# Kernel tuning notes

Hardware: AMD Instinct MI355X
Metric: run time of the kernel (lower is better)

Reference implementation:

```python
import jax, jax.numpy as jnp
import numpy as np

N = 100000          # active sites
C_IN = 256          # inplanes == outplanes
C_MID = 64          # innerplanes
K = 9               # 3x3 kernel offsets (2D)


def setup_inputs() -> dict:
    key = jax.random.key(0)
    ks = jax.random.split(key, 12)
    features = jax.random.normal(ks[0], (N, C_IN), dtype=jnp.float32)
    # submanifold rulebook: for each active site, index of active neighbor per
    # kernel offset; sentinel N = no active neighbor, center (offset 4) = self
    idx = jax.random.randint(ks[1], (N, K), 0, N, dtype=jnp.int32)
    drop = jax.random.uniform(ks[2], (N, K)) < 0.3
    idx = jnp.where(drop, jnp.int32(N), idx)
    neighbor_idx = idx.at[:, 4].set(jnp.arange(N, dtype=jnp.int32))
    s = 0.05
    return {
        "features": features,
        "neighbor_idx": neighbor_idx,
        "w1": jax.random.normal(ks[3], (C_IN, C_MID), dtype=jnp.float32) * s,
        "scale1": jnp.ones((C_MID,), jnp.float32),
        "bias1": jnp.zeros((C_MID,), jnp.float32),
        "w2": jax.random.normal(ks[4], (K, C_MID, C_MID), dtype=jnp.float32) * s,
        "scale2": jnp.ones((C_MID,), jnp.float32),
        "bias2": jnp.zeros((C_MID,), jnp.float32),
        "w3": jax.random.normal(ks[5], (C_MID, C_IN), dtype=jnp.float32) * s,
        "scale3": jnp.ones((C_IN,), jnp.float32),
        "bias3": jnp.zeros((C_IN,), jnp.float32),
    }


def reference(features, neighbor_idx, w1, scale1, bias1, w2, scale2, bias2,
              w3, scale3, bias3):
    # conv1: 1x1 submanifold conv == per-site matmul; affine BN; ReLU
    out = jax.nn.relu(features @ w1 * scale1 + bias1)            # [N, C_MID]
    # conv2: 3x3 submanifold conv via rulebook gather-matmul-accumulate
    padded = jnp.concatenate([out, jnp.zeros((1, C_MID), out.dtype)], axis=0)
    gathered = padded[neighbor_idx]                               # [N, K, C_MID]
    out = jnp.einsum('nkc,kcd->nd', gathered, w2)                 # [N, C_MID]
    out = jax.nn.relu(out * scale2 + bias2)
    # conv3: 1x1 conv; affine BN; residual add (downsample=None); ReLU
    out = out @ w3 * scale3 + bias3 + features                    # [N, C_IN]
    return jax.nn.relu(out)
```

## Files before the change

kernel.cpp:

```cpp
#include <hip/hip_runtime.h>
#include <stdint.h>

#define C_IN 256
#define C_MID 64
#define KOFF 9

typedef __attribute__((ext_vector_type(8))) short bf16x8;
typedef __attribute__((ext_vector_type(4))) short short4v;
typedef __attribute__((ext_vector_type(4))) float f32x4;
typedef __attribute__((ext_vector_type(4))) float float4v;

__device__ inline unsigned short f2bf(float f) {
    union { float f; unsigned u; } x; x.f = f;
    unsigned r = x.u + 0x7FFFu + ((x.u >> 16) & 1u);
    return (unsigned short)(r >> 16);
}

__global__ void prep_kernel(const float* __restrict__ w1, const float* __restrict__ s1,
                            const float* __restrict__ w2, const float* __restrict__ s2,
                            const float* __restrict__ w3, const float* __restrict__ s3,
                            unsigned short* __restrict__ w1t,
                            unsigned short* __restrict__ w2t,
                            unsigned short* __restrict__ w3t,
                            unsigned short* __restrict__ zrow) {
    int tid = blockIdx.x * blockDim.x + threadIdx.x;
    int stride = gridDim.x * blockDim.x;
    for (int i = tid; i < C_MID * C_IN; i += stride) {
        int n = i / C_IN, k = i % C_IN;
        w1t[i] = f2bf(w1[k * C_MID + n] * s1[n]);
    }
    for (int i = tid; i < KOFF * C_MID * C_MID; i += stride) {
        int k = i / (C_MID * C_MID);
        int r = i % (C_MID * C_MID);
        int d = r / C_MID, c = r % C_MID;
        w2t[i] = f2bf(w2[(k * C_MID + c) * C_MID + d] * s2[d]);
    }
    for (int i = tid; i < C_IN * C_MID; i += stride) {
        int e = i / C_MID, c = i % C_MID;
        w3t[i] = f2bf(w3[c * C_IN + e] * s3[e]);
    }
    for (int i = tid; i < C_MID; i += stride) zrow[i] = 0;
}

__global__ __launch_bounds__(256, 4) void conv1_kernel(
    const float* __restrict__ feat, const unsigned short* __restrict__ w1t,
    const float* __restrict__ b1, unsigned short* __restrict__ out1, int N)
{
    __shared__ __align__(16) unsigned short sW1[16384];

    int t = threadIdx.x;
    int wave = t >> 6;
    int lane = t & 63;
    int l15 = lane & 15;
    int quad = lane >> 4;
    int row_tile = blockIdx.x * 64;
    int site = row_tile + wave * 16 + l15;
    int sitec = site < N ? site : (N - 1);

    const bf16x8* w1c = reinterpret_cast<const bf16x8*>(w1t);
    bf16x8* sW1c = reinterpret_cast<bf16x8*>(sW1);
#pragma unroll
    for (int it = 0; it < 8; ++it) {
        int s = it * 256 + t;
        int l = s & 15, ct = (s >> 4) & 3, q = (s >> 6) & 3, kk = s >> 8;
        sW1c[s] = w1c[(ct * 16 + l) * 32 + kk * 4 + q];
    }

    float4v fr[16];
#pragma unroll
    for (int kk = 0; kk < 8; ++kk) {
        const float4v* p = reinterpret_cast<const float4v*>(
            feat + (size_t)sitec * C_IN + kk * 32 + quad * 8);
        fr[kk * 2] = p[0];
        fr[kk * 2 + 1] = p[1];
    }
    __builtin_amdgcn_sched_barrier(0);
    __syncthreads();

    f32x4 acc[4] = {};
#pragma unroll
    for (int kk = 0; kk < 8; ++kk) {
        union { unsigned short s[8]; bf16x8 v; } ua;
#pragma unroll
        for (int j = 0; j < 4; ++j) {
            ua.s[j] = f2bf(fr[kk * 2][j]);
            ua.s[4 + j] = f2bf(fr[kk * 2 + 1][j]);
        }
#pragma unroll
        for (int ct = 0; ct < 4; ++ct) {
            bf16x8 fa = sW1c[((kk * 4 + quad) * 4 + ct) * 16 + l15];
            acc[ct] = __builtin_amdgcn_mfma_f32_16x16x32_bf16(fa, ua.v, acc[ct], 0, 0, 0);
        }
    }
    if (site < N) {
#pragma unroll
        for (int ct = 0; ct < 4; ++ct) {
            const float4v* bp = reinterpret_cast<const float4v*>(b1 + ct * 16 + quad * 4);
            float4v bb = bp[0];
            union { unsigned short s[4]; short4v v; } o;
#pragma unroll
            for (int reg = 0; reg < 4; ++reg)
                o.s[reg] = f2bf(fmaxf(acc[ct][reg] + bb[reg], 0.f));
            *reinterpret_cast<short4v*>(out1 + (size_t)site * C_MID + ct * 16 + quad * 4) = o.v;
        }
    }
}

__global__ __launch_bounds__(256, 2) void conv23_kernel(
    const float* __restrict__ feat, const int* __restrict__ nbr,
    const unsigned short* __restrict__ out1, const unsigned short* __restrict__ w2t,
    const float* __restrict__ b2, const unsigned short* __restrict__ w3t,
    const float* __restrict__ b3, float* __restrict__ out, int N)
{
    __shared__ __align__(16) unsigned short sWB[36864];
    __shared__ int sNbr[64 * KOFF];

    int t = threadIdx.x;
    int wave = t >> 6;
    int lane = t & 63;
    int l15 = lane & 15;
    int quad = lane >> 4;
    int row_tile = blockIdx.x * 64;
    int site = row_tile + wave * 16 + l15;
    int sitec = site < N ? site : (N - 1);

    bf16x8* sWBc = reinterpret_cast<bf16x8*>(sWB);

    const bf16x8* w2c = reinterpret_cast<const bf16x8*>(w2t);
#pragma unroll
    for (int it = 0; it < 18; ++it) {
        int s = it * 256 + t;
        int l = s & 15, ct = (s >> 4) & 3, q = (s >> 6) & 3, kk = (s >> 8) & 1, k = s >> 9;
        sWBc[s] = w2c[k * 512 + (ct * 16 + l) * 8 + kk * 4 + q];
    }
#pragma unroll
    for (int i = 0; i < 3; ++i) {
        int j = i * 256 + t;
        if (j < 64 * KOFF) {
            int g = row_tile * KOFF + j;
            sNbr[j] = (g < N * KOFF) ? nbr[g] : N;
        }
    }
    __syncthreads();

    int rt = wave * 16 + l15;
    int nb[KOFF];
#pragma unroll
    for (int k = 0; k < KOFF; ++k) nb[k] = sNbr[rt * KOFF + k];

    bf16x8 ga[KOFF][2];
#pragma unroll
    for (int k = 0; k < KOFF; ++k) {
        const bf16x8* pg = reinterpret_cast<const bf16x8*>(out1 + (size_t)nb[k] * C_MID + quad * 8);
        ga[k][0] = pg[0];
        ga[k][1] = pg[4];
    }
    float4v rf[16];
#pragma unroll
    for (int c2 = 0; c2 < 16; ++c2)
        rf[c2] = *reinterpret_cast<const float4v*>(
            feat + (size_t)sitec * C_IN + c2 * 16 + quad * 4);
    __builtin_amdgcn_sched_barrier(0);

    f32x4 acc2[4] = {};
#pragma unroll
    for (int k = 0; k < KOFF; ++k) {
#pragma unroll
        for (int kk = 0; kk < 2; ++kk) {
#pragma unroll
            for (int ct = 0; ct < 4; ++ct) {
                bf16x8 fa = sWBc[((k * 2 + kk) * 4 + quad) * 64 + ct * 16 + l15];
                acc2[ct] = __builtin_amdgcn_mfma_f32_16x16x32_bf16(fa, ga[k][kk], acc2[ct], 0, 0, 0);
            }
        }
    }
    __syncthreads();

    unsigned short* mid = &sWB[31744];
#pragma unroll
    for (int ct = 0; ct < 4; ++ct) {
        const float4v* bp = reinterpret_cast<const float4v*>(b2 + ct * 16 + quad * 4);
        float4v bb = bp[0];
        union { unsigned short s[4]; short4v v; } o;
#pragma unroll
        for (int reg = 0; reg < 4; ++reg)
            o.s[reg] = f2bf(fmaxf(acc2[ct][reg] + bb[reg], 0.f));
        *reinterpret_cast<short4v*>(&mid[(wave * 16 + l15) * 80 + ct * 16 + quad * 4]) = o.v;
    }
    const bf16x8* w3c = reinterpret_cast<const bf16x8*>(w3t);
#pragma unroll
    for (int it = 0; it < 8; ++it) {
        int s = it * 256 + t;
        int l = s & 15, c2 = (s >> 4) & 15, q = (s >> 8) & 3, kk = (s >> 10) & 1;
        sWBc[s] = w3c[(c2 * 16 + l) * 8 + kk * 4 + q];
    }
    __syncthreads();

    f32x4 acc3[16] = {};
#pragma unroll
    for (int kk = 0; kk < 2; ++kk) {
        bf16x8 fb = *reinterpret_cast<const bf16x8*>(
            &mid[(wave * 16 + l15) * 80 + kk * 32 + quad * 8]);
#pragma unroll
        for (int c2 = 0; c2 < 16; ++c2) {
            bf16x8 fa = sWBc[((kk * 4 + quad) * 16 + c2) * 16 + l15];
            acc3[c2] = __builtin_amdgcn_mfma_f32_16x16x32_bf16(fa, fb, acc3[c2], 0, 0, 0);
        }
    }
    if (site < N) {
#pragma unroll
        for (int c2 = 0; c2 < 16; ++c2) {
            const float4v* bp = reinterpret_cast<const float4v*>(b3 + c2 * 16 + quad * 4);
            float4v bb = bp[0];
            float4v o;
#pragma unroll
            for (int reg = 0; reg < 4; ++reg)
                o[reg] = fmaxf(acc3[c2][reg] + bb[reg] + rf[c2][reg], 0.f);
            *reinterpret_cast<float4v*>(out + (size_t)site * C_IN + c2 * 16 + quad * 4) = o;
        }
    }
}

extern "C" void kernel_launch(void* const* d_in, const int* in_sizes, int n_in,
                              void* d_out, int out_size, void* d_ws, size_t ws_size,
                              hipStream_t stream) {
    const float* feat = (const float*)d_in[0];
    const int*   nbr  = (const int*)d_in[1];
    const float* w1   = (const float*)d_in[2];
    const float* s1   = (const float*)d_in[3];
    const float* b1   = (const float*)d_in[4];
    const float* w2   = (const float*)d_in[5];
    const float* s2   = (const float*)d_in[6];
    const float* b2   = (const float*)d_in[7];
    const float* w3   = (const float*)d_in[8];
    const float* s3   = (const float*)d_in[9];
    const float* b3   = (const float*)d_in[10];
    float* out = (float*)d_out;
    int N = in_sizes[0] / C_IN;

    char* ws = (char*)d_ws;
    unsigned short* w1t  = (unsigned short*)(ws);
    unsigned short* w2t  = (unsigned short*)(ws + 32768);
    unsigned short* w3t  = (unsigned short*)(ws + 32768 + 73728);
    unsigned short* out1 = (unsigned short*)(ws + 139264);

    prep_kernel<<<80, 256, 0, stream>>>(w1, s1, w2, s2, w3, s3, w1t, w2t, w3t,
                                        out1 + (size_t)N * C_MID);
    int nblk = (N + 63) / 64;
    conv1_kernel<<<nblk, 256, 0, stream>>>(feat, w1t, b1, out1, N);
    conv23_kernel<<<nblk, 256, 0, stream>>>(feat, nbr, out1, w2t, b2, w3t, b3, out, N);
}
```

Measured before the change: 263.8 us.

## Double conv23 block size and split conv3 into halves to cut register pressure

The conv23 kernel now processes 128 sites per 512-thread block, so the 72KB shared weight load is amortized over twice as many sites. Residual feature loads are split in two halves, and conv3 accumulation is done in two 8-tile passes, to lower live registers and allow launch_bounds(512,4). The mid buffer moves to a smaller-stride region. The risk is spilling or lower occupancy if the register target cannot be met, and larger blocks make tail effects coarser.

```diff
diff --git a/kernel.cpp b/kernel.cpp
--- a/kernel.cpp
+++ b/kernel.cpp
@@ -106,44 +106,43 @@
     }
 }
 
-__global__ __launch_bounds__(256, 2) void conv23_kernel(
+__global__ __launch_bounds__(512, 4) void conv23_kernel(
     const float* __restrict__ feat, const int* __restrict__ nbr,
     const unsigned short* __restrict__ out1, const unsigned short* __restrict__ w2t,
     const float* __restrict__ b2, const unsigned short* __restrict__ w3t,
     const float* __restrict__ b3, float* __restrict__ out, int N)
 {
     __shared__ __align__(16) unsigned short sWB[36864];
-    __shared__ int sNbr[64 * KOFF];
+    __shared__ int sNbr[128 * KOFF];
 
     int t = threadIdx.x;
     int wave = t >> 6;
     int lane = t & 63;
     int l15 = lane & 15;
     int quad = lane >> 4;
-    int row_tile = blockIdx.x * 64;
-    int site = row_tile + wave * 16 + l15;
+    int rt = wave * 16 + l15;
+    int site = blockIdx.x * 128 + rt;
     int sitec = site < N ? site : (N - 1);
 
     bf16x8* sWBc = reinterpret_cast<bf16x8*>(sWB);
 
     const bf16x8* w2c = reinterpret_cast<const bf16x8*>(w2t);
 #pragma unroll
-    for (int it = 0; it < 18; ++it) {
-        int s = it * 256 + t;
+    for (int it = 0; it < 9; ++it) {
+        int s = it * 512 + t;
         int l = s & 15, ct = (s >> 4) & 3, q = (s >> 6) & 3, kk = (s >> 8) & 1, k = s >> 9;
         sWBc[s] = w2c[k * 512 + (ct * 16 + l) * 8 + kk * 4 + q];
     }
 #pragma unroll
     for (int i = 0; i < 3; ++i) {
-        int j = i * 256 + t;
-        if (j < 64 * KOFF) {
-            int g = row_tile * KOFF + j;
+        int j = i * 512 + t;
+        if (j < 128 * KOFF) {
+            int g = blockIdx.x * 128 * KOFF + j;
             sNbr[j] = (g < N * KOFF) ? nbr[g] : N;
         }
     }
     __syncthreads();
 
-    int rt = wave * 16 + l15;
     int nb[KOFF];
 #pragma unroll
     for (int k = 0; k < KOFF; ++k) nb[k] = sNbr[rt * KOFF + k];
@@ -155,11 +154,6 @@
         ga[k][0] = pg[0];
         ga[k][1] = pg[4];
     }
-    float4v rf[16];
-#pragma unroll
-    for (int c2 = 0; c2 < 16; ++c2)
-        rf[c2] = *reinterpret_cast<const float4v*>(
-            feat + (size_t)sitec * C_IN + c2 * 16 + quad * 4);
     __builtin_amdgcn_sched_barrier(0);
 
     f32x4 acc2[4] = {};
@@ -174,49 +168,73 @@
             }
         }
     }
-    __syncthreads();
-
-    unsigned short* mid = &sWB[31744];
+    float4v b2r[4];
+#pragma unroll
+    for (int ct = 0; ct < 4; ++ct)
+        b2r[ct] = *reinterpret_cast<const float4v*>(b2 + ct * 16 + quad * 4);
+    float4v rfA[8], b3A[8];
+#pragma unroll
+    for (int c8 = 0; c8 < 8; ++c8) {
+        rfA[c8] = *reinterpret_cast<const float4v*>(
+            feat + (size_t)sitec * C_IN + c8 * 16 + quad * 4);
+        b3A[c8] = *reinterpret_cast<const float4v*>(b3 + c8 * 16 + quad * 4);
+    }
+    __builtin_amdgcn_sched_barrier(0);
+    __syncthreads();
+
+    unsigned short* mid = &sWB[16384];
 #pragma unroll
     for (int ct = 0; ct < 4; ++ct) {
-        const float4v* bp = reinterpret_cast<const float4v*>(b2 + ct * 16 + quad * 4);
-        float4v bb = bp[0];
         union { unsigned short s[4]; short4v v; } o;
 #pragma unroll
         for (int reg = 0; reg < 4; ++reg)
-            o.s[reg] = f2bf(fmaxf(acc2[ct][reg] + bb[reg], 0.f));
-        *reinterpret_cast<short4v*>(&mid[(wave * 16 + l15) * 80 + ct * 16 + quad * 4]) = o.v;
+            o.s[reg] = f2bf(fmaxf(acc2[ct][reg] + b2r[ct][reg], 0.f));
+        *reinterpret_cast<short4v*>(&mid[rt * 72 + ct * 16 + quad * 4]) = o.v;
     }
     const bf16x8* w3c = reinterpret_cast<const bf16x8*>(w3t);
 #pragma unroll
-    for (int it = 0; it < 8; ++it) {
-        int s = it * 256 + t;
+    for (int it = 0; it < 4; ++it) {
+        int s = it * 512 + t;
         int l = s & 15, c2 = (s >> 4) & 15, q = (s >> 8) & 3, kk = (s >> 10) & 1;
         sWBc[s] = w3c[(c2 * 16 + l) * 8 + kk * 4 + q];
     }
     __syncthreads();
 
-    f32x4 acc3[16] = {};
-#pragma unroll
-    for (int kk = 0; kk < 2; ++kk) {
-        bf16x8 fb = *reinterpret_cast<const bf16x8*>(
-            &mid[(wave * 16 + l15) * 80 + kk * 32 + quad * 8]);
-#pragma unroll
-        for (int c2 = 0; c2 < 16; ++c2) {
-            bf16x8 fa = sWBc[((kk * 4 + quad) * 16 + c2) * 16 + l15];
-            acc3[c2] = __builtin_amdgcn_mfma_f32_16x16x32_bf16(fa, fb, acc3[c2], 0, 0, 0);
-        }
-    }
-    if (site < N) {
-#pragma unroll
-        for (int c2 = 0; c2 < 16; ++c2) {
-            const float4v* bp = reinterpret_cast<const float4v*>(b3 + c2 * 16 + quad * 4);
-            float4v bb = bp[0];
-            float4v o;
-#pragma unroll
-            for (int reg = 0; reg < 4; ++reg)
-                o[reg] = fmaxf(acc3[c2][reg] + bb[reg] + rf[c2][reg], 0.f);
-            *reinterpret_cast<float4v*>(out + (size_t)site * C_IN + c2 * 16 + quad * 4) = o;
+    float4v rfB[8], b3B[8];
+#pragma unroll
+    for (int c8 = 0; c8 < 8; ++c8) {
+        rfB[c8] = *reinterpret_cast<const float4v*>(
+            feat + (size_t)sitec * C_IN + (8 + c8) * 16 + quad * 4);
+        b3B[c8] = *reinterpret_cast<const float4v*>(b3 + (8 + c8) * 16 + quad * 4);
+    }
+    __builtin_amdgcn_sched_barrier(0);
+
+#pragma unroll
+    for (int half = 0; half < 2; ++half) {
+        f32x4 acc3[8] = {};
+#pragma unroll
+        for (int kk = 0; kk < 2; ++kk) {
+            bf16x8 fb = *reinterpret_cast<const bf16x8*>(
+                &mid[rt * 72 + kk * 32 + quad * 8]);
+#pragma unroll
+            for (int c8 = 0; c8 < 8; ++c8) {
+                int c2 = half * 8 + c8;
+                bf16x8 fa = sWBc[((kk * 4 + quad) * 16 + c2) * 16 + l15];
+                acc3[c8] = __builtin_amdgcn_mfma_f32_16x16x32_bf16(fa, fb, acc3[c8], 0, 0, 0);
+            }
+        }
+        if (site < N) {
+#pragma unroll
+            for (int c8 = 0; c8 < 8; ++c8) {
+                int c2 = half * 8 + c8;
+                float4v bb = half ? b3B[c8] : b3A[c8];
+                float4v rr = half ? rfB[c8] : rfA[c8];
+                float4v o;
+#pragma unroll
+                for (int reg = 0; reg < 4; ++reg)
+                    o[reg] = fmaxf(acc3[c8][reg] + bb[reg] + rr[reg], 0.f);
+                *reinterpret_cast<float4v*>(out + (size_t)site * C_IN + c2 * 16 + quad * 4) = o;
+            }
         }
     }
 }
@@ -246,7 +264,6 @@
 
     prep_kernel<<<80, 256, 0, stream>>>(w1, s1, w2, s2, w3, s3, w1t, w2t, w3t,
                                         out1 + (size_t)N * C_MID);
-    int nblk = (N + 63) / 64;
-    conv1_kernel<<<nblk, 256, 0, stream>>>(feat, w1t, b1, out1, N);
-    conv23_kernel<<<nblk, 256, 0, stream>>>(feat, nbr, out1, w2t, b2, w3t, b3, out, N);
-}
+    conv1_kernel<<<(N + 63) / 64, 256, 0, stream>>>(feat, w1t, b1, out1, N);
+    conv23_kernel<<<(N + 127) / 128, 512, 0, stream>>>(feat, nbr, out1, w2t, b2, w3t, b3, out, N);
+}
```

Result: slower. 287.9 us (+9.1%).

## Split conv2 weight staging into two LDS phases and defer residual loads

Applied to the files above, without the earlier changes.

The conv23 kernel now stages the 3x3 weights in two chunks (offsets 0-4, then 5-8) so the shared buffer shrinks from about 72KB to about 42KB. The aim is to allow more blocks per CU. The residual feature loads move after the conv2 MMAs to cut register pressure during the gather/MMA phase, and conv1 splits its feature loads into two halves. In exchange it adds extra syncthreads and a second global weight load per block, and the mid tile padding changes from 80 to 72.

```diff
diff --git a/kernel.cpp b/kernel.cpp
--- a/kernel.cpp
+++ b/kernel.cpp
@@ -53,8 +53,7 @@
     int lane = t & 63;
     int l15 = lane & 15;
     int quad = lane >> 4;
-    int row_tile = blockIdx.x * 64;
-    int site = row_tile + wave * 16 + l15;
+    int site = blockIdx.x * 64 + wave * 16 + l15;
     int sitec = site < N ? site : (N - 1);
 
     const bf16x8* w1c = reinterpret_cast<const bf16x8*>(w1t);
@@ -66,25 +65,35 @@
         sW1c[s] = w1c[(ct * 16 + l) * 32 + kk * 4 + q];
     }
 
-    float4v fr[16];
-#pragma unroll
-    for (int kk = 0; kk < 8; ++kk) {
+    float4v fr0[8];
+#pragma unroll
+    for (int kk = 0; kk < 4; ++kk) {
         const float4v* p = reinterpret_cast<const float4v*>(
             feat + (size_t)sitec * C_IN + kk * 32 + quad * 8);
-        fr[kk * 2] = p[0];
-        fr[kk * 2 + 1] = p[1];
-    }
-    __builtin_amdgcn_sched_barrier(0);
-    __syncthreads();
+        fr0[kk * 2] = p[0];
+        fr0[kk * 2 + 1] = p[1];
+    }
+    __builtin_amdgcn_sched_barrier(0);
+    __syncthreads();
+
+    float4v fr1[8];
+#pragma unroll
+    for (int kk = 0; kk < 4; ++kk) {
+        const float4v* p = reinterpret_cast<const float4v*>(
+            feat + (size_t)sitec * C_IN + (kk + 4) * 32 + quad * 8);
+        fr1[kk * 2] = p[0];
+        fr1[kk * 2 + 1] = p[1];
+    }
+    __builtin_amdgcn_sched_barrier(0);
 
     f32x4 acc[4] = {};
 #pragma unroll
-    for (int kk = 0; kk < 8; ++kk) {
+    for (int kk = 0; kk < 4; ++kk) {
         union { unsigned short s[8]; bf16x8 v; } ua;
 #pragma unroll
         for (int j = 0; j < 4; ++j) {
-            ua.s[j] = f2bf(fr[kk * 2][j]);
-            ua.s[4 + j] = f2bf(fr[kk * 2 + 1][j]);
+            ua.s[j] = f2bf(fr0[kk * 2][j]);
+            ua.s[4 + j] = f2bf(fr0[kk * 2 + 1][j]);
         }
 #pragma unroll
         for (int ct = 0; ct < 4; ++ct) {
@@ -92,11 +101,24 @@
             acc[ct] = __builtin_amdgcn_mfma_f32_16x16x32_bf16(fa, ua.v, acc[ct], 0, 0, 0);
         }
     }
+#pragma unroll
+    for (int kk = 0; kk < 4; ++kk) {
+        union { unsigned short s[8]; bf16x8 v; } ua;
+#pragma unroll
+        for (int j = 0; j < 4; ++j) {
+            ua.s[j] = f2bf(fr1[kk * 2][j]);
+            ua.s[4 + j] = f2bf(fr1[kk * 2 + 1][j]);
+        }
+#pragma unroll
+        for (int ct = 0; ct < 4; ++ct) {
+            bf16x8 fa = sW1c[(((kk + 4) * 4 + quad) * 4 + ct) * 16 + l15];
+            acc[ct] = __builtin_amdgcn_mfma_f32_16x16x32_bf16(fa, ua.v, acc[ct], 0, 0, 0);
+        }
+    }
     if (site < N) {
 #pragma unroll
         for (int ct = 0; ct < 4; ++ct) {
-            const float4v* bp = reinterpret_cast<const float4v*>(b1 + ct * 16 + quad * 4);
-            float4v bb = bp[0];
+            float4v bb = *reinterpret_cast<const float4v*>(b1 + ct * 16 + quad * 4);
             union { unsigned short s[4]; short4v v; } o;
 #pragma unroll
             for (int reg = 0; reg < 4; ++reg)
@@ -112,7 +134,7 @@
     const float* __restrict__ b2, const unsigned short* __restrict__ w3t,
     const float* __restrict__ b3, float* __restrict__ out, int N)
 {
-    __shared__ __align__(16) unsigned short sWB[36864];
+    __shared__ __align__(16) unsigned short sWB[21504];
     __shared__ int sNbr[64 * KOFF];
 
     int t = threadIdx.x;
@@ -120,15 +142,15 @@
     int lane = t & 63;
     int l15 = lane & 15;
     int quad = lane >> 4;
-    int row_tile = blockIdx.x * 64;
-    int site = row_tile + wave * 16 + l15;
+    int rt = wave * 16 + l15;
+    int site = blockIdx.x * 64 + rt;
     int sitec = site < N ? site : (N - 1);
 
     bf16x8* sWBc = reinterpret_cast<bf16x8*>(sWB);
-
     const bf16x8* w2c = reinterpret_cast<const bf16x8*>(w2t);
-#pragma unroll
-    for (int it = 0; it < 18; ++it) {
+
+#pragma unroll
+    for (int it = 0; it < 10; ++it) {
         int s = it * 256 + t;
         int l = s & 15, ct = (s >> 4) & 3, q = (s >> 6) & 3, kk = (s >> 8) & 1, k = s >> 9;
         sWBc[s] = w2c[k * 512 + (ct * 16 + l) * 8 + kk * 4 + q];
@@ -137,13 +159,12 @@
     for (int i = 0; i < 3; ++i) {
         int j = i * 256 + t;
         if (j < 64 * KOFF) {
-            int g = row_tile * KOFF + j;
+            int g = blockIdx.x * 64 * KOFF + j;
             sNbr[j] = (g < N * KOFF) ? nbr[g] : N;
         }
     }
     __syncthreads();
 
-    int rt = wave * 16 + l15;
     int nb[KOFF];
 #pragma unroll
     for (int k = 0; k < KOFF; ++k) nb[k] = sNbr[rt * KOFF + k];
@@ -155,16 +176,11 @@
         ga[k][0] = pg[0];
         ga[k][1] = pg[4];
     }
-    float4v rf[16];
-#pragma unroll
-    for (int c2 = 0; c2 < 16; ++c2)
-        rf[c2] = *reinterpret_cast<const float4v*>(
-            feat + (size_t)sitec * C_IN + c2 * 16 + quad * 4);
     __builtin_amdgcn_sched_barrier(0);
 
     f32x4 acc2[4] = {};
 #pragma unroll
-    for (int k = 0; k < KOFF; ++k) {
+    for (int k = 0; k < 5; ++k) {
 #pragma unroll
         for (int kk = 0; kk < 2; ++kk) {
 #pragma unroll
@@ -176,16 +192,42 @@
     }
     __syncthreads();
 
-    unsigned short* mid = &sWB[31744];
+#pragma unroll
+    for (int it = 0; it < 8; ++it) {
+        int s = it * 256 + t;
+        int l = s & 15, ct = (s >> 4) & 3, q = (s >> 6) & 3, kk = (s >> 8) & 1, k2 = s >> 9;
+        sWBc[s] = w2c[(5 + k2) * 512 + (ct * 16 + l) * 8 + kk * 4 + q];
+    }
+    __syncthreads();
+#pragma unroll
+    for (int k = 5; k < KOFF; ++k) {
+        int kloc = k - 5;
+#pragma unroll
+        for (int kk = 0; kk < 2; ++kk) {
+#pragma unroll
+            for (int ct = 0; ct < 4; ++ct) {
+                bf16x8 fa = sWBc[((kloc * 2 + kk) * 4 + quad) * 64 + ct * 16 + l15];
+                acc2[ct] = __builtin_amdgcn_mfma_f32_16x16x32_bf16(fa, ga[k][kk], acc2[ct], 0, 0, 0);
+            }
+        }
+    }
+    float4v rf[16];
+#pragma unroll
+    for (int c2 = 0; c2 < 16; ++c2)
+        rf[c2] = *reinterpret_cast<const float4v*>(
+            feat + (size_t)sitec * C_IN + c2 * 16 + quad * 4);
+    __builtin_amdgcn_sched_barrier(0);
+    __syncthreads();
+
+    unsigned short* mid = &sWB[16384];
 #pragma unroll
     for (int ct = 0; ct < 4; ++ct) {
-        const float4v* bp = reinterpret_cast<const float4v*>(b2 + ct * 16 + quad * 4);
-        float4v bb = bp[0];
+        float4v bb = *reinterpret_cast<const float4v*>(b2 + ct * 16 + quad * 4);
         union { unsigned short s[4]; short4v v; } o;
 #pragma unroll
         for (int reg = 0; reg < 4; ++reg)
             o.s[reg] = f2bf(fmaxf(acc2[ct][reg] + bb[reg], 0.f));
-        *reinterpret_cast<short4v*>(&mid[(wave * 16 + l15) * 80 + ct * 16 + quad * 4]) = o.v;
+        *reinterpret_cast<short4v*>(&mid[rt * 72 + ct * 16 + quad * 4]) = o.v;
     }
     const bf16x8* w3c = reinterpret_cast<const bf16x8*>(w3t);
 #pragma unroll
@@ -200,7 +242,7 @@
 #pragma unroll
     for (int kk = 0; kk < 2; ++kk) {
         bf16x8 fb = *reinterpret_cast<const bf16x8*>(
-            &mid[(wave * 16 + l15) * 80 + kk * 32 + quad * 8]);
+            &mid[rt * 72 + kk * 32 + quad * 8]);
 #pragma unroll
         for (int c2 = 0; c2 < 16; ++c2) {
             bf16x8 fa = sWBc[((kk * 4 + quad) * 16 + c2) * 16 + l15];
@@ -210,8 +252,7 @@
     if (site < N) {
 #pragma unroll
         for (int c2 = 0; c2 < 16; ++c2) {
-            const float4v* bp = reinterpret_cast<const float4v*>(b3 + c2 * 16 + quad * 4);
-            float4v bb = bp[0];
+            float4v bb = *reinterpret_cast<const float4v*>(b3 + c2 * 16 + quad * 4);
             float4v o;
 #pragma unroll
             for (int reg = 0; reg < 4; ++reg)
```

Result: no change. 261.6 us (-0.8%).
